# Kernel optimization log

Hardware: AMD Instinct MI355X
Metric: run time of the kernel (lower is better)

## Reference

```python
import jax, jax.numpy as jnp
import numpy as np

N = 500000      # number of active voxels (same coords in/out: stride 1)
C_IN = 32
C_OUT = 32
K = 27          # 3x3x3 kernel volume
M = 250000      # neighbors per kernel offset (fixed for jit-ability)


def setup_inputs() -> dict:
    key = jax.random.key(0)
    k1, k2, k3, k4 = jax.random.split(key, 4)
    feats = jax.random.normal(k1, (N, C_IN), dtype=jnp.float32)
    std = 1.0 / np.sqrt(C_IN * K)
    weight = jax.random.uniform(k2, (K, C_IN, C_OUT), dtype=jnp.float32,
                                minval=-std, maxval=std)
    in_idx = jax.random.randint(k3, (K, M), 0, N, dtype=jnp.int32)
    out_idx = jax.random.randint(k4, (K, M), 0, N, dtype=jnp.int32)
    return {"feats": feats, "weight": weight, "in_idx": in_idx, "out_idx": out_idx}


def reference(feats, weight, in_idx, out_idx):
    # gather: [K, M, C_in]
    gathered = feats[in_idx]
    # per-offset matmul: [K, M, C_out]
    edge_out = jnp.einsum('kmc,kcd->kmd', gathered, weight)
    # scatter-add into output rows: [N, C_out]
    out = jnp.zeros((feats.shape[0], weight.shape[-1]), dtype=feats.dtype)
    out = out.at[out_idx.reshape(-1)].add(edge_out.reshape(-1, weight.shape[-1]))
    return out
```

## Files before the change

kernel.cpp:

```cpp
#include <hip/hip_runtime.h>

#define C_IN   32
#define C_OUT  32
#define K_VOL  27
#define M_EDGE 250000
#define N_ROWS 500000
#define E_TOT  (K_VOL * M_EDGE)

#define NT        (N_ROWS / 16)
#define NREG      977
#define BPB       16
#define CHUNK     (M_EDGE / BPB)
#define OSTRIDE   (NREG + 1)
#define NSEG      (K_VOL * BPB)
#define NLISTS    512
#define CAPL      16
#define LSTRIDE   17

typedef __attribute__((ext_vector_type(8))) short s16x8;
typedef __attribute__((ext_vector_type(4))) float f32x4;

static __device__ __forceinline__ unsigned short f2bf(float x) {
    union { float f; unsigned int u; } c; c.f = x;
    const unsigned int r = (c.u + 0x7FFFu + ((c.u >> 16) & 1u)) >> 16;
    return (unsigned short)r;
}
static __device__ __forceinline__ unsigned int cvtpk(float lo, float hi) {
    unsigned int r;
    asm("v_cvt_pk_bf16_f32 %0, %1, %2" : "=v"(r) : "v"(lo), "v"(hi));
    return r;
}
static __device__ __forceinline__ void unpack_add(float2* af, const s16x8& f) {
    union { s16x8 v; unsigned int w[4]; } u; u.v = f;
#pragma unroll
    for (int d = 0; d < 4; ++d) {
        af[d].x += __uint_as_float(u.w[d] << 16);
        af[d].y += __uint_as_float(u.w[d] & 0xffff0000u);
    }
}

__global__ __launch_bounds__(256) void cvt_feats(
    const float* __restrict__ f, unsigned short* __restrict__ o)
{
    const int i = blockIdx.x * 256 + threadIdx.x;
    if (i >= N_ROWS * C_IN / 8) return;
    const float4 v0 = reinterpret_cast<const float4*>(f)[i * 2];
    const float4 v1 = reinterpret_cast<const float4*>(f)[i * 2 + 1];
    s16x8 r;
    r[0] = (short)f2bf(v0.x); r[1] = (short)f2bf(v0.y);
    r[2] = (short)f2bf(v0.z); r[3] = (short)f2bf(v0.w);
    r[4] = (short)f2bf(v1.x); r[5] = (short)f2bf(v1.y);
    r[6] = (short)f2bf(v1.z); r[7] = (short)f2bf(v1.w);
    *reinterpret_cast<s16x8*>(o + (size_t)i * 8) = r;
}

__global__ __launch_bounds__(256) void cvt_w(
    const float* __restrict__ w, unsigned short* __restrict__ wT)
{
    const int idx = blockIdx.x * 256 + threadIdx.x;
    if (idx >= K_VOL * C_IN * C_OUT) return;
    const int k = idx >> 10, rem = idx & 1023;
    const int co = rem >> 5, ci = rem & 31;
    wT[idx] = f2bf(w[k * 1024 + ci * 32 + co]);
}

__global__ __launch_bounds__(256) void fill3_kernel(
    const int* __restrict__ in_idx, const int* __restrict__ out_idx,
    int* __restrict__ lstartG, unsigned int* __restrict__ edge_buf)
{
    __shared__ int lh[NREG];
    __shared__ int lstart[NREG + 1];
    __shared__ int lcur[NREG];
    __shared__ int partial[256];
    __shared__ unsigned int pay[CHUNK];
    const int blk = blockIdx.x, k = blockIdx.y, tid = threadIdx.x;
    const int seg = k * BPB + blk;

    for (int r = tid; r < NREG; r += 256) lh[r] = 0;
    __syncthreads();

    const int eb0 = k * M_EDGE + blk * CHUNK;
    const int* ob = out_idx + eb0;
    const int* ib = in_idx + eb0;

    for (int t = tid; t < CHUNK; t += 256)
        atomicAdd(&lh[ob[t] >> 9], 1);
    __syncthreads();

    int psum = 0;
    const int r0 = tid * 4;
#pragma unroll
    for (int j = 0; j < 4; ++j) { const int r = r0 + j; if (r < NREG) psum += lh[r]; }
    partial[tid] = psum;
    __syncthreads();
    for (int off = 1; off < 256; off <<= 1) {
        const int t = (tid >= off) ? partial[tid - off] : 0;
        __syncthreads();
        partial[tid] += t;
        __syncthreads();
    }
    int run = partial[tid] - psum;
#pragma unroll
    for (int j = 0; j < 4; ++j) {
        const int r = r0 + j;
        if (r < NREG) { lstart[r] = run; lcur[r] = run; run += lh[r]; }
    }
    if (tid == 0) lstart[NREG] = CHUNK;
    __syncthreads();

    for (int r = tid; r <= NREG; r += 256)
        lstartG[seg * OSTRIDE + r] = lstart[r];

    for (int t = tid; t < CHUNK; t += 256) {
        const int row = ob[t];
        const int irow = ib[t];
        const int idx = atomicAdd(&lcur[row >> 9], 1);
        pay[idx] = (unsigned int)irow | ((unsigned int)(row & 15) << 19) |
                   ((unsigned int)((row >> 4) & 31) << 23);
    }
    __syncthreads();

    unsigned int* dst = edge_buf + (size_t)seg * CHUNK;
    for (int q = tid; q < CHUNK; q += 256)
        dst[q] = pay[q];
}

__global__ __launch_bounds__(512, 4) void conv_mfma9(
    const unsigned short* __restrict__ feats16,
    const unsigned short* __restrict__ wT16,
    const int* __restrict__ lstartG,
    const unsigned int* __restrict__ edge_buf,
    float* __restrict__ out)
{
    __shared__ int lcnt[NLISTS];
    __shared__ unsigned int lists[NLISTS * LSTRIDE];
    __shared__ int offsh[2 * BPB];
    const int g = blockIdx.x;
    const int tid = threadIdx.x;
    const int lane = tid & 63, wv = tid >> 6;
    const int slot = lane & 15, chunk = lane >> 4;

    f32x4 a0[4], a1[4];
#pragma unroll
    for (int j = 0; j < 4; ++j) {
        a0[j] = (f32x4){0.f, 0.f, 0.f, 0.f};
        a1[j] = (f32x4){0.f, 0.f, 0.f, 0.f};
    }

#pragma unroll 1
    for (int k = 0; k < K_VOL; ++k) {
        lcnt[tid] = 0;
        if (tid < 2 * BPB)
            offsh[tid] = lstartG[(k * BPB + (tid >> 1)) * OSTRIDE + g + (tid & 1)];
        __syncthreads();

        const int bb = tid >> 5, u = tid & 31;
        const int sB = offsh[2 * bb], eB = offsh[2 * bb + 1];
        const unsigned int* ebp = edge_buf + (size_t)(k * BPB + bb) * CHUNK;
        for (int t = sB + u; t < eB; t += 32) {
            const unsigned int p = ebp[t];
            const int li = (int)((p >> 19) & 0x1FFu);
            const int idx = atomicAdd(&lcnt[li], 1);
            if (idx < CAPL) lists[li * LSTRIDE + idx] = p & 0x7FFFFu;
        }
        __syncthreads();

        const unsigned short* wk = wT16 + k * (C_IN * C_OUT);
        const s16x8 b0 = *reinterpret_cast<const s16x8*>(wk + slot * 32 + chunk * 8);
        const s16x8 b1 = *reinterpret_cast<const s16x8*>(wk + (slot + 16) * 32 + chunk * 8);

        int myc[4]; unsigned int e0[4], e1[4];
#pragma unroll
        for (int j = 0; j < 4; ++j) {
            const int li = (wv * 4 + j) * 16 + slot;
            const int c = lcnt[li];
            myc[j] = c > CAPL ? CAPL : c;
            e0[j] = lists[li * LSTRIDE];
            e1[j] = lists[li * LSTRIDE + 1];
        }
        s16x8 g0[4], g1[4];
#pragma unroll
        for (int j = 0; j < 4; ++j) {
            g0[j] = (s16x8){0, 0, 0, 0, 0, 0, 0, 0};
            g1[j] = (s16x8){0, 0, 0, 0, 0, 0, 0, 0};
        }
#pragma unroll
        for (int j = 0; j < 4; ++j)
            if (0 < myc[j])
                g0[j] = *reinterpret_cast<const s16x8*>(
                    feats16 + (size_t)e0[j] * C_IN + chunk * 8);
#pragma unroll
        for (int j = 0; j < 4; ++j)
            if (1 < myc[j])
                g1[j] = *reinterpret_cast<const s16x8*>(
                    feats16 + (size_t)e1[j] * C_IN + chunk * 8);

#pragma unroll
        for (int j = 0; j < 4; ++j) {
            float2 af[4];
#pragma unroll
            for (int d = 0; d < 4; ++d) af[d] = make_float2(0.f, 0.f);
            unpack_add(af, g0[j]);
            unpack_add(af, g1[j]);
            const int li = (wv * 4 + j) * 16 + slot;
#pragma unroll 1
            for (int i = 2; __any(i < myc[j]); ++i) {
                s16x8 f = {0, 0, 0, 0, 0, 0, 0, 0};
                if (i < myc[j])
                    f = *reinterpret_cast<const s16x8*>(
                        feats16 + (size_t)lists[li * LSTRIDE + i] * C_IN + chunk * 8);
                unpack_add(af, f);
            }
            union { unsigned int w[4]; s16x8 v; } A;
#pragma unroll
            for (int d = 0; d < 4; ++d) A.w[d] = cvtpk(af[d].x, af[d].y);
            a0[j] = __builtin_amdgcn_mfma_f32_16x16x32_bf16(A.v, b0, a0[j], 0, 0, 0);
            a1[j] = __builtin_amdgcn_mfma_f32_16x16x32_bf16(A.v, b1, a1[j], 0, 0, 0);
        }
        __syncthreads();
    }

#pragma unroll
    for (int j = 0; j < 4; ++j) {
        const int rtg = g * 32 + wv * 4 + j;
        if (rtg < NT) {
            const int r0 = rtg * 16 + chunk * 4;
#pragma unroll
            for (int jj = 0; jj < 4; ++jj) {
                out[(size_t)(r0 + jj) * C_OUT + slot]      = a0[j][jj];
                out[(size_t)(r0 + jj) * C_OUT + 16 + slot] = a1[j][jj];
            }
        }
    }
}

__global__ __launch_bounds__(256) void spconv_edges(
    const float* __restrict__ feats, const float* __restrict__ weight,
    const int* __restrict__ in_idx, const int* __restrict__ out_idx,
    float* __restrict__ out)
{
    const int k = blockIdx.y;
    const int tid = threadIdx.x;
    const int g = tid >> 3, l = tid & 7, c0 = l * 4;
    const float* wk = weight + k * (C_IN * C_OUT);
    float4 wr[32];
#pragma unroll
    for (int ci = 0; ci < 32; ++ci)
        wr[ci] = *reinterpret_cast<const float4*>(wk + ci * C_OUT + c0);
    const int* ik = in_idx + k * M_EDGE;
    const int* ok = out_idx + k * M_EDGE;
    int m = blockIdx.x * 1024 + g;
#pragma unroll 1
    for (int it = 0; it < 32; ++it, m += 32) {
        if (m >= M_EDGE) break;
        const int irow = ik[m], orow = ok[m];
        const float4* frow =
            reinterpret_cast<const float4*>(feats + (size_t)irow * C_IN);
        float4 a = make_float4(0.f, 0.f, 0.f, 0.f);
#pragma unroll
        for (int j = 0; j < 8; ++j) {
            const float4 f4 = frow[j];
            const float fv[4] = {f4.x, f4.y, f4.z, f4.w};
#pragma unroll
            for (int t = 0; t < 4; ++t) {
                const float4 w4 = wr[j * 4 + t];
                a.x = fmaf(fv[t], w4.x, a.x);
                a.y = fmaf(fv[t], w4.y, a.y);
                a.z = fmaf(fv[t], w4.z, a.z);
                a.w = fmaf(fv[t], w4.w, a.w);
            }
        }
        float* op = out + (size_t)orow * C_OUT + c0;
        unsafeAtomicAdd(op + 0, a.x);
        unsafeAtomicAdd(op + 1, a.y);
        unsafeAtomicAdd(op + 2, a.z);
        unsafeAtomicAdd(op + 3, a.w);
    }
}

extern "C" void kernel_launch(void* const* d_in, const int* in_sizes, int n_in,
                              void* d_out, int out_size, void* d_ws, size_t ws_size,
                              hipStream_t stream) {
    const float* feats   = (const float*)d_in[0];
    const float* weight  = (const float*)d_in[1];
    const int*   in_idx  = (const int*)d_in[2];
    const int*   out_idx = (const int*)d_in[3];
    float*       out     = (float*)d_out;

    const size_t feats16_elems = (size_t)N_ROWS * C_IN;
    const size_t wT16_elems    = (size_t)K_VOL * C_IN * C_OUT;
    const size_t lstart_elems  = (size_t)NSEG * OSTRIDE;
    const size_t need_bytes = feats16_elems * 2 + wT16_elems * 2 +
        lstart_elems * sizeof(int) + (size_t)E_TOT * 4 + 256;

    if (ws_size >= need_bytes) {
        unsigned short* feats16 = (unsigned short*)d_ws;
        unsigned short* wT16    = feats16 + feats16_elems;
        int* lstartG = (int*)(wT16 + wT16_elems);
        unsigned int* edge_buf = (unsigned int*)(lstartG + lstart_elems);

        cvt_feats<<<(N_ROWS * C_IN / 8 + 255) / 256, 256, 0, stream>>>(feats, feats16);
        cvt_w<<<(K_VOL * C_IN * C_OUT + 255) / 256, 256, 0, stream>>>(weight, wT16);
        fill3_kernel<<<dim3(BPB, K_VOL), 256, 0, stream>>>(in_idx, out_idx,
                                                           lstartG, edge_buf);
        conv_mfma9<<<NREG, 512, 0, stream>>>(feats16, wT16, lstartG, edge_buf, out);
    } else {
        hipMemsetAsync(out, 0, (size_t)out_size * sizeof(float), stream);
        dim3 grid((M_EDGE + 1023) / 1024, K_VOL);
        spconv_edges<<<grid, dim3(256), 0, stream>>>(feats, weight, in_idx, out_idx, out);
    }
}
```

Before: 294.3 us.

## Fuse feature/weight conversion into bucketing prep kernel and preload segment offsets

```diff
diff --git a/kernel.cpp b/kernel.cpp
--- a/kernel.cpp
+++ b/kernel.cpp
@@ -17,6 +17,10 @@
 #define CAPL      16
 #define LSTRIDE   17
 
+#define NCVT      2048
+#define NI_F      (N_ROWS * C_IN / 8)
+#define NI_W      (K_VOL * C_IN * C_OUT)
+
 typedef __attribute__((ext_vector_type(8))) short s16x8;
 typedef __attribute__((ext_vector_type(4))) float f32x4;
 
@@ -39,33 +43,10 @@
     }
 }
 
-__global__ __launch_bounds__(256) void cvt_feats(
-    const float* __restrict__ f, unsigned short* __restrict__ o)
-{
-    const int i = blockIdx.x * 256 + threadIdx.x;
-    if (i >= N_ROWS * C_IN / 8) return;
-    const float4 v0 = reinterpret_cast<const float4*>(f)[i * 2];
-    const float4 v1 = reinterpret_cast<const float4*>(f)[i * 2 + 1];
-    s16x8 r;
-    r[0] = (short)f2bf(v0.x); r[1] = (short)f2bf(v0.y);
-    r[2] = (short)f2bf(v0.z); r[3] = (short)f2bf(v0.w);
-    r[4] = (short)f2bf(v1.x); r[5] = (short)f2bf(v1.y);
-    r[6] = (short)f2bf(v1.z); r[7] = (short)f2bf(v1.w);
-    *reinterpret_cast<s16x8*>(o + (size_t)i * 8) = r;
-}
-
-__global__ __launch_bounds__(256) void cvt_w(
-    const float* __restrict__ w, unsigned short* __restrict__ wT)
-{
-    const int idx = blockIdx.x * 256 + threadIdx.x;
-    if (idx >= K_VOL * C_IN * C_OUT) return;
-    const int k = idx >> 10, rem = idx & 1023;
-    const int co = rem >> 5, ci = rem & 31;
-    wT[idx] = f2bf(w[k * 1024 + ci * 32 + co]);
-}
-
-__global__ __launch_bounds__(256) void fill3_kernel(
+__global__ __launch_bounds__(256) void prep_kernel(
+    const float* __restrict__ feats, const float* __restrict__ weight,
     const int* __restrict__ in_idx, const int* __restrict__ out_idx,
+    unsigned short* __restrict__ feats16, unsigned short* __restrict__ wT16,
     int* __restrict__ lstartG, unsigned int* __restrict__ edge_buf)
 {
     __shared__ int lh[NREG];
@@ -73,7 +54,30 @@
     __shared__ int lcur[NREG];
     __shared__ int partial[256];
     __shared__ unsigned int pay[CHUNK];
-    const int blk = blockIdx.x, k = blockIdx.y, tid = threadIdx.x;
+    const int bx = blockIdx.x, tid = threadIdx.x;
+
+    if (bx >= NSEG) {
+        const int id0 = (bx - NSEG) * 256 + tid;
+        const int stride = NCVT * 256;
+        for (int i = id0; i < NI_F; i += stride) {
+            const float4 v0 = reinterpret_cast<const float4*>(feats)[i * 2];
+            const float4 v1 = reinterpret_cast<const float4*>(feats)[i * 2 + 1];
+            s16x8 r;
+            r[0] = (short)f2bf(v0.x); r[1] = (short)f2bf(v0.y);
+            r[2] = (short)f2bf(v0.z); r[3] = (short)f2bf(v0.w);
+            r[4] = (short)f2bf(v1.x); r[5] = (short)f2bf(v1.y);
+            r[6] = (short)f2bf(v1.z); r[7] = (short)f2bf(v1.w);
+            *reinterpret_cast<s16x8*>(feats16 + (size_t)i * 8) = r;
+        }
+        if (id0 < NI_W) {
+            const int k = id0 >> 10, rem = id0 & 1023;
+            const int co = rem >> 5, ci = rem & 31;
+            wT16[id0] = f2bf(weight[k * 1024 + ci * 32 + co]);
+        }
+        return;
+    }
+
+    const int blk = bx & 15, k = bx >> 4;
     const int seg = k * BPB + blk;
 
     for (int r = tid; r < NREG; r += 256) lh[r] = 0;
@@ -125,7 +129,7 @@
         dst[q] = pay[q];
 }
 
-__global__ __launch_bounds__(512, 4) void conv_mfma9(
+__global__ __launch_bounds__(512, 4) void conv_mfma11(
     const unsigned short* __restrict__ feats16,
     const unsigned short* __restrict__ wT16,
     const int* __restrict__ lstartG,
@@ -134,12 +138,15 @@
 {
     __shared__ int lcnt[NLISTS];
     __shared__ unsigned int lists[NLISTS * LSTRIDE];
-    __shared__ int offsh[2 * BPB];
+    __shared__ int lsAll[NSEG * 2];
     const int g = blockIdx.x;
     const int tid = threadIdx.x;
     const int lane = tid & 63, wv = tid >> 6;
     const int slot = lane & 15, chunk = lane >> 4;
 
+    for (int i = tid; i < NSEG * 2; i += 512)
+        lsAll[i] = lstartG[(i >> 1) * OSTRIDE + g + (i & 1)];
+
     f32x4 a0[4], a1[4];
 #pragma unroll
     for (int j = 0; j < 4; ++j) {
@@ -150,12 +157,10 @@
 #pragma unroll 1
     for (int k = 0; k < K_VOL; ++k) {
         lcnt[tid] = 0;
-        if (tid < 2 * BPB)
-            offsh[tid] = lstartG[(k * BPB + (tid >> 1)) * OSTRIDE + g + (tid & 1)];
         __syncthreads();
 
         const int bb = tid >> 5, u = tid & 31;
-        const int sB = offsh[2 * bb], eB = offsh[2 * bb + 1];
+        const int sB = lsAll[(k * BPB + bb) * 2], eB = lsAll[(k * BPB + bb) * 2 + 1];
         const unsigned int* ebp = edge_buf + (size_t)(k * BPB + bb) * CHUNK;
         for (int t = sB + u; t < eB; t += 32) {
             const unsigned int p = ebp[t];
@@ -299,11 +304,9 @@
         int* lstartG = (int*)(wT16 + wT16_elems);
         unsigned int* edge_buf = (unsigned int*)(lstartG + lstart_elems);
 
-        cvt_feats<<<(N_ROWS * C_IN / 8 + 255) / 256, 256, 0, stream>>>(feats, feats16);
-        cvt_w<<<(K_VOL * C_IN * C_OUT + 255) / 256, 256, 0, stream>>>(weight, wT16);
-        fill3_kernel<<<dim3(BPB, K_VOL), 256, 0, stream>>>(in_idx, out_idx,
-                                                           lstartG, edge_buf);
-        conv_mfma9<<<NREG, 512, 0, stream>>>(feats16, wT16, lstartG, edge_buf, out);
+        prep_kernel<<<NSEG + NCVT, 256, 0, stream>>>(
+            feats, weight, in_idx, out_idx, feats16, wT16, lstartG, edge_buf);
+        conv_mfma11<<<NREG, 512, 0, stream>>>(feats16, wT16, lstartG, edge_buf, out);
     } else {
         hipMemsetAsync(out, 0, (size_t)out_size * sizeof(float), stream);
         dim3 grid((M_EDGE + 1023) / 1024, K_VOL);
```

New measurement: 263.4 us. 10.5% less time.
